# Kernel optimization log

Measured on AMD Instinct MI355X. Metric: run time of the kernel, lower is better.

Reference implementation:

```python
import jax, jax.numpy as jnp
import numpy as np

B, DIN, DOUT, K = 2048, 2048, 2048, 16

def setup_inputs() -> dict:
    key = jax.random.key(0)
    k1, k2, k3 = jax.random.split(key, 3)
    # init scale from reset_parameters: s = 3**0.5 / ((din+dout)/2 * k)**0.25
    d = (DIN + DOUT) / 2.0
    s = 3.0 ** 0.5 / (d * K) ** 0.25
    x = jax.random.normal(k1, (B, DIN), dtype=jnp.float32)
    w1 = jax.random.uniform(k2, (DIN, DOUT, K), minval=-s, maxval=s, dtype=jnp.float32)
    w2 = jax.random.uniform(k3, (DIN, DOUT, K), minval=-s, maxval=s, dtype=jnp.float32)
    b1 = jnp.zeros((DOUT, K), dtype=jnp.float32)
    b2 = jnp.zeros((DOUT,), dtype=jnp.float32)
    return {"x": x, "w1": w1, "b1": b1, "w2": w2, "b2": b2}

def reference(x, w1, b1, w2, b2):
    # g: [b, o, k] gating mixture, relu-activated
    g = jax.nn.relu(jnp.einsum('bi,iok->bok', x, w1) + b1)
    # three-way contraction over i and k -> [b, o]
    out = jnp.einsum('bi,iok,bok->bo', x, w2, g) + b2
    return out
```

## Files before the change

### kernel.cpp

```cpp
#include <hip/hip_runtime.h>
#include <hip/hip_bf16.h>


typedef __bf16 bf16;
typedef bf16 bf16x8 __attribute__((ext_vector_type(8)));
typedef bf16 bf16x4 __attribute__((ext_vector_type(4)));
typedef float f32x4 __attribute__((ext_vector_type(4)));

typedef __attribute__((address_space(1))) const void gco_void;
typedef __attribute__((address_space(3))) void lds_void;

#define DIN_   2048
#define DOUT_  2048
#define NP_    32768

__device__ __forceinline__ bf16x8 cvt8(f32x4 a, f32x4 b) {
    bf16x8 v;
    v[0] = (bf16)a[0]; v[1] = (bf16)a[1]; v[2] = (bf16)a[2]; v[3] = (bf16)a[3];
    v[4] = (bf16)b[0]; v[5] = (bf16)b[1]; v[6] = (bf16)b[2]; v[7] = (bf16)b[3];
    return v;
}

__global__ __launch_bounds__(256)
void xcvt(const float* __restrict__ x, bf16* __restrict__ xb) {
    const size_t i = ((size_t)blockIdx.x * 256 + threadIdx.x) * 8;
    f32x4 a = *(const f32x4*)(x + i);
    f32x4 b = *(const f32x4*)(x + i + 4);
    *(bf16x8*)(xb + i) = cvt8(a, b);
}

__global__ __launch_bounds__(256)
void wtrans(const float* __restrict__ w1, const float* __restrict__ w2,
            bf16* __restrict__ w1t, bf16* __restrict__ w2t) {
    __shared__ float s[64][65];
    const int t  = threadIdx.x;
    const int lr = t >> 4;
    const int lq = t & 15;
    const int n0 = blockIdx.x * 64;
    const int i0 = blockIdx.y * 64;
    const float* src = blockIdx.z ? w2 : w1;
    bf16*        dst = blockIdx.z ? w2t : w1t;
#pragma unroll
    for (int r = 0; r < 4; ++r) {
        const int il = lr + 16 * r;
        f32x4 v = *(const f32x4*)(src + (size_t)(i0 + il) * NP_ + n0 + lq * 4);
        s[il][lq * 4 + 0] = v[0]; s[il][lq * 4 + 1] = v[1];
        s[il][lq * 4 + 2] = v[2]; s[il][lq * 4 + 3] = v[3];
    }
    __syncthreads();
#pragma unroll
    for (int r = 0; r < 4; ++r) {
        const int nl = lr + 16 * r;
        bf16x4 o;
        o[0] = (bf16)s[lq * 4 + 0][nl]; o[1] = (bf16)s[lq * 4 + 1][nl];
        o[2] = (bf16)s[lq * 4 + 2][nl]; o[3] = (bf16)s[lq * 4 + 3][nl];
        *(bf16x4*)(dst + (size_t)(n0 + nl) * DIN_ + i0 + lq * 4) = o;
    }
}

__global__ __launch_bounds__(1024, 1)
void mix2_gemm16w(const bf16* __restrict__ xb, const bf16* __restrict__ w1t,
                  const bf16* __restrict__ w2t, const float* __restrict__ b1,
                  const float* __restrict__ b2, float* __restrict__ out)
{
    __shared__ alignas(16) char lds[131072];

    const int tid  = threadIdx.x;
    const int lane = tid & 63;
    const int wid  = tid >> 6;
    const int wm   = wid >> 2;
    const int wn   = wid & 3;
    const int lk   = lane & 15;
    const int lg   = lane >> 4;

    const int nwg = gridDim.x;
    const int bid = (blockIdx.x & 7) * (nwg >> 3) + (blockIdx.x >> 3);
    const int mt  = bid & 7;
    const int nt  = bid >> 3;

    const int arow = tid >> 2;
    const int aswz = ((tid & 3) ^ ((arow >> 1) & 3)) * 8;
    const int tb   = tid & 511;
    const int brow = tb >> 2;
    const int bswz = ((tb & 3) ^ ((brow >> 1) & 3)) * 8;
    const bf16* gA = xb + (size_t)(mt * 256 + arow) * DIN_ + aswz;
    const bf16* gB = (tid < 512 ? w1t : w2t) + (size_t)(nt * 128 + brow) * DIN_ + bswz;
    const int adst = arow * 64 + (tid & 3) * 16;
    const int bdst = 16384 + (tid >= 512 ? 8192 : 0) + tb * 16;

    const int kswz = (lg ^ ((lk >> 1) & 3)) * 16;
    int aoff[4], boff[2];
#pragma unroll
    for (int fm = 0; fm < 4; ++fm) aoff[fm] = (wm * 64 + fm * 16 + lk) * 64 + kswz;
#pragma unroll
    for (int fn = 0; fn < 2; ++fn) boff[fn] = 16384 + (wn * 32 + fn * 16 + lk) * 64 + kswz;

    f32x4 acc1[4][2], acc2[4][2];
#pragma unroll
    for (int i = 0; i < 4; ++i)
#pragma unroll
        for (int j = 0; j < 2; ++j) {
            acc1[i][j] = (f32x4){0.f, 0.f, 0.f, 0.f};
            acc2[i][j] = (f32x4){0.f, 0.f, 0.f, 0.f};
        }

    auto STG = [&](int h) {
        char* r = lds + (h & 3) * 32768;
        const int koff = h * 32;
        __builtin_amdgcn_global_load_lds((gco_void*)(gA + koff), (lds_void*)(r + adst), 16, 0, 0);
        __builtin_amdgcn_global_load_lds((gco_void*)(gB + koff), (lds_void*)(r + bdst), 16, 0, 0);
    };

    auto PHASE = [&](int h) {
        const char* r = lds + (h & 3) * 32768;
        bf16x8 a[4], u[2], v[2];
#pragma unroll
        for (int fn = 0; fn < 2; ++fn) {
            u[fn] = *(const bf16x8*)(r + boff[fn]);
            v[fn] = *(const bf16x8*)(r + boff[fn] + 8192);
        }
#pragma unroll
        for (int fm = 0; fm < 4; ++fm) a[fm] = *(const bf16x8*)(r + aoff[fm]);
        __builtin_amdgcn_s_setprio(1);
#pragma unroll
        for (int fm = 0; fm < 4; ++fm)
#pragma unroll
            for (int fn = 0; fn < 2; ++fn) {
                acc1[fm][fn] = __builtin_amdgcn_mfma_f32_16x16x32_bf16(a[fm], u[fn], acc1[fm][fn], 0, 0, 0);
                acc2[fm][fn] = __builtin_amdgcn_mfma_f32_16x16x32_bf16(a[fm], v[fn], acc2[fm][fn], 0, 0, 0);
            }
        __builtin_amdgcn_s_setprio(0);
    };

#define SYNC(W) do { asm volatile("s_waitcnt vmcnt(" #W ")" ::: "memory"); \
    __builtin_amdgcn_s_barrier(); __builtin_amdgcn_sched_barrier(0); } while (0)

    STG(0); STG(1); STG(2);

#pragma unroll 1
    for (int t = 0; t < 15; ++t) {
        const int h0 = t * 4;
#pragma unroll
        for (int q = 0; q < 4; ++q) {
            SYNC(4);
            STG(h0 + q + 3);
            PHASE(h0 + q);
        }
    }
    SYNC(4); STG(63); PHASE(60);
    SYNC(4);          PHASE(61);
    SYNC(2);          PHASE(62);
    SYNC(0);          PHASE(63);

#undef SYNC

    const int obase = nt * 8 + wn * 2;
#pragma unroll
    for (int fn = 0; fn < 2; ++fn) {
        const int o = obase + fn;
        const float bb1 = b1[(size_t)o * 16 + lk];
        const float bb2 = b2[o];
#pragma unroll
        for (int fm = 0; fm < 4; ++fm) {
#pragma unroll
            for (int j = 0; j < 4; ++j) {
                float g = fmaxf(acc1[fm][fn][j] + bb1, 0.f);
                float p = g * acc2[fm][fn][j];
                p += __shfl_xor(p, 1);
                p += __shfl_xor(p, 2);
                p += __shfl_xor(p, 4);
                p += __shfl_xor(p, 8);
                if (lk == 0) {
                    const int brow2 = mt * 256 + wm * 64 + fm * 16 + lg * 4 + j;
                    out[(size_t)brow2 * DOUT_ + o] = p + bb2;
                }
            }
        }
    }
}

__global__ __launch_bounds__(512)
void mix2_fused_direct(const float* __restrict__ x, const float* __restrict__ w1,
                       const float* __restrict__ b1, const float* __restrict__ w2,
                       const float* __restrict__ b2, float* __restrict__ out)
{
    __shared__ alignas(16) char lds[2 * 49152];

    const int tid  = threadIdx.x;
    const int lane = tid & 63;
    const int wid  = tid >> 6;
    const int wm   = wid >> 2;
    const int wn   = wid & 3;

    const int nwg = gridDim.x;
    const int bid = (blockIdx.x & 7) * (nwg >> 3) + (blockIdx.x >> 3);
    const int mt  = bid & 15;
    const int nt  = bid >> 4;

    const int lk  = lane & 15;
    const int lg  = lane >> 4;
    const int swz = (lane & 7) << 4;

    const int a_row  = tid >> 3;
    const int a_col8 = tid & 7;
    const int b_ib = ((tid >> 5) & 15) << 2;
    const int b_nb = (tid & 31) << 2;

    const float* pa  = x  + (size_t)(mt * 128 + a_row) * DIN_ + a_col8 * 8;
    const float* pb1 = w1 + (size_t)b_ib * NP_ + (size_t)nt * 128 + b_nb;
    const float* pb2 = w2 + (size_t)b_ib * NP_ + (size_t)nt * 128 + b_nb;

    const int aswz   = (a_col8 * 16) ^ ((a_row & 7) << 4);
    const int aoffw0 = a_row * 128 + aswz;
    const int aoffw1 = (a_row + 64) * 128 + aswz;

    int aoff[4], boff1[2], boff2[2];
#pragma unroll
    for (int fm = 0; fm < 4; ++fm) aoff[fm] = (wm * 64 + fm * 16 + lk) * 128;
#pragma unroll
    for (int fn = 0; fn < 2; ++fn) {
        const int n = wn * 32 + fn * 16 + lk;
        boff1[fn] = 16384 + n * 128;
        boff2[fn] = 32768 + n * 128;
    }
    const int kp0 = (lg * 16) ^ swz;
    const int kp1 = (64 + lg * 16) ^ swz;

    f32x4 acc1[4][2], acc2[4][2];
#pragma unroll
    for (int i = 0; i < 4; ++i)
#pragma unroll
        for (int j = 0; j < 2; ++j) {
            acc1[i][j] = (f32x4){0.f, 0.f, 0.f, 0.f};
            acc2[i][j] = (f32x4){0.f, 0.f, 0.f, 0.f};
        }

    f32x4 rA[4], rB1[4], rB2[4];

    auto LOAD = [&](int kt) {
        const float* a0 = pa + kt * 64;
        rA[0] = *(const f32x4*)(a0);
        rA[1] = *(const f32x4*)(a0 + 4);
        rA[2] = *(const f32x4*)(a0 + (size_t)64 * DIN_);
        rA[3] = *(const f32x4*)(a0 + (size_t)64 * DIN_ + 4);
        const float* q1 = pb1 + (size_t)kt * 64 * NP_;
        const float* q2 = pb2 + (size_t)kt * 64 * NP_;
#pragma unroll
        for (int j = 0; j < 4; ++j) {
            rB1[j] = *(const f32x4*)(q1 + (size_t)j * NP_);
            rB2[j] = *(const f32x4*)(q2 + (size_t)j * NP_);
        }
    };

    auto STORE = [&](char* s) {
        *(bf16x8*)(s + aoffw0) = cvt8(rA[0], rA[1]);
        *(bf16x8*)(s + aoffw1) = cvt8(rA[2], rA[3]);
        char* s1 = s + 16384;
        char* s2 = s + 32768;
#pragma unroll
        for (int c = 0; c < 4; ++c) {
            const int n   = b_nb + c;
            const int off = n * 128 + ((b_ib * 2) ^ ((n & 7) << 4));
            bf16x4 v1, v2;
            v1[0] = (bf16)rB1[0][c]; v1[1] = (bf16)rB1[1][c];
            v1[2] = (bf16)rB1[2][c]; v1[3] = (bf16)rB1[3][c];
            v2[0] = (bf16)rB2[0][c]; v2[1] = (bf16)rB2[1][c];
            v2[2] = (bf16)rB2[2][c]; v2[3] = (bf16)rB2[3][c];
            *(bf16x4*)(s1 + off) = v1;
            *(bf16x4*)(s2 + off) = v2;
        }
    };

    auto COMPUTE = [&](const char* s) {
#pragma unroll
        for (int kb = 0; kb < 2; ++kb) {
            const int kp = kb ? kp1 : kp0;
            bf16x8 a[4], u[2], v[2];
#pragma unroll
            for (int fm = 0; fm < 4; ++fm) a[fm] = *(const bf16x8*)(s + aoff[fm] + kp);
#pragma unroll
            for (int fn = 0; fn < 2; ++fn) u[fn] = *(const bf16x8*)(s + boff1[fn] + kp);
#pragma unroll
            for (int fn = 0; fn < 2; ++fn) v[fn] = *(const bf16x8*)(s + boff2[fn] + kp);
#pragma unroll
            for (int fm = 0; fm < 4; ++fm)
#pragma unroll
                for (int fn = 0; fn < 2; ++fn) {
                    acc1[fm][fn] = __builtin_amdgcn_mfma_f32_16x16x32_bf16(a[fm], u[fn], acc1[fm][fn], 0, 0, 0);
                    acc2[fm][fn] = __builtin_amdgcn_mfma_f32_16x16x32_bf16(a[fm], v[fn], acc2[fm][fn], 0, 0, 0);
                }
        }
    };

    char* buf0 = lds;
    char* buf1 = lds + 49152;

    LOAD(0);
    STORE(buf0);
    __syncthreads();

    for (int kt = 0; kt < 32; ++kt) {
        if (kt + 1 < 32) LOAD(kt + 1);
        COMPUTE((kt & 1) ? buf1 : buf0);
        if (kt + 1 < 32) {
            STORE((kt & 1) ? buf0 : buf1);
            __syncthreads();
        }
    }

    const int obase = nt * 8 + wn * 2;
#pragma unroll
    for (int fn = 0; fn < 2; ++fn) {
        const int o = obase + fn;
        const float bb1 = b1[(size_t)o * 16 + lk];
        const float bb2 = b2[o];
#pragma unroll
        for (int fm = 0; fm < 4; ++fm) {
#pragma unroll
            for (int j = 0; j < 4; ++j) {
                float g = fmaxf(acc1[fm][fn][j] + bb1, 0.f);
                float p = g * acc2[fm][fn][j];
                p += __shfl_xor(p, 1);
                p += __shfl_xor(p, 2);
                p += __shfl_xor(p, 4);
                p += __shfl_xor(p, 8);
                if (lk == 0) {
                    const int brow = mt * 128 + wm * 64 + fm * 16 + lg * 4 + j;
                    out[(size_t)brow * DOUT_ + o] = p + bb2;
                }
            }
        }
    }
}

extern "C" void kernel_launch(void* const* d_in, const int* in_sizes, int n_in,
                              void* d_out, int out_size, void* d_ws, size_t ws_size,
                              hipStream_t stream) {
    (void)in_sizes; (void)n_in; (void)out_size;
    const float* x  = (const float*)d_in[0];
    const float* w1 = (const float*)d_in[1];
    const float* b1 = (const float*)d_in[2];
    const float* w2 = (const float*)d_in[3];
    const float* b2 = (const float*)d_in[4];
    float* out = (float*)d_out;

    const size_t XB   = (size_t)DIN_ * DIN_ * 2;
    const size_t WT   = (size_t)NP_ * DIN_ * 2;
    const size_t NEED = XB + 2 * WT;

    if (ws_size >= NEED) {
        bf16* xb  = (bf16*)d_ws;
        bf16* w1t = (bf16*)((char*)d_ws + XB);
        bf16* w2t = (bf16*)((char*)d_ws + XB + WT);
        hipLaunchKernelGGL(xcvt,   dim3(2048),        dim3(256),  0, stream, x, xb);
        hipLaunchKernelGGL(wtrans, dim3(512, 32, 2),  dim3(256),  0, stream, w1, w2, w1t, w2t);
        hipLaunchKernelGGL(mix2_gemm16w, dim3(2048),  dim3(1024), 0, stream, xb, w1t, w2t, b1, b2, out);
    } else {
        hipLaunchKernelGGL(mix2_fused_direct, dim3(4096), dim3(512), 0, stream, x, w1, b1, w2, b2, out);
    }
}
```

Baseline: 642.8 us.

## Switch GEMM pipeline to double-buffered 64-wide K stages with full waits

Replaces the 4-stage ring of 32-wide K tiles (prefetch depth 3, partial vmcnt waits) with a 2-buffer scheme of 64-wide K tiles, each thread issuing four global-to-LDS loads per stage. It also uses a new 8-way XOR swizzle for the 128-byte rows. The goal is half as many barriers and more MFMA work per synchronisation. In exchange, prefetch depth drops to one stage and every stage waits on vmcnt(0), which may expose more memory latency.

```diff
diff --git a/kernel.cpp b/kernel.cpp
--- a/kernel.cpp
+++ b/kernel.cpp
@@ -59,9 +59,9 @@
 }
 
 __global__ __launch_bounds__(1024, 1)
-void mix2_gemm16w(const bf16* __restrict__ xb, const bf16* __restrict__ w1t,
-                  const bf16* __restrict__ w2t, const float* __restrict__ b1,
-                  const float* __restrict__ b2, float* __restrict__ out)
+void mix2_gemm2b(const bf16* __restrict__ xb, const bf16* __restrict__ w1t,
+                 const bf16* __restrict__ w2t, const float* __restrict__ b1,
+                 const float* __restrict__ b2, float* __restrict__ out)
 {
     __shared__ alignas(16) char lds[131072];
 
@@ -78,22 +78,28 @@
     const int mt  = bid & 7;
     const int nt  = bid >> 3;
 
-    const int arow = tid >> 2;
-    const int aswz = ((tid & 3) ^ ((arow >> 1) & 3)) * 8;
-    const int tb   = tid & 511;
-    const int brow = tb >> 2;
-    const int bswz = ((tb & 3) ^ ((brow >> 1) & 3)) * 8;
-    const bf16* gA = xb + (size_t)(mt * 256 + arow) * DIN_ + aswz;
-    const bf16* gB = (tid < 512 ? w1t : w2t) + (size_t)(nt * 128 + brow) * DIN_ + bswz;
-    const int adst = arow * 64 + (tid & 3) * 16;
-    const int bdst = 16384 + (tid >= 512 ? 8192 : 0) + tb * 16;
-
-    const int kswz = (lg ^ ((lk >> 1) & 3)) * 16;
-    int aoff[4], boff[2];
-#pragma unroll
-    for (int fm = 0; fm < 4; ++fm) aoff[fm] = (wm * 64 + fm * 16 + lk) * 64 + kswz;
-#pragma unroll
-    for (int fn = 0; fn < 2; ++fn) boff[fn] = 16384 + (wn * 32 + fn * 16 + lk) * 64 + kswz;
+    const int srow = tid >> 3;
+    const int sswz = ((tid & 7) ^ (srow & 7)) * 8;
+    const bf16* gA0 = xb  + (size_t)(mt * 256 + srow) * DIN_ + sswz;
+    const bf16* gA1 = gA0 + (size_t)128 * DIN_;
+    const bf16* gB1 = w1t + (size_t)(nt * 128 + srow) * DIN_ + sswz;
+    const bf16* gB2 = w2t + (size_t)(nt * 128 + srow) * DIN_ + sswz;
+
+    int aoff[4][2], boff[2][2];
+#pragma unroll
+    for (int fm = 0; fm < 4; ++fm)
+#pragma unroll
+        for (int h2 = 0; h2 < 2; ++h2) {
+            const int row = wm * 64 + fm * 16 + lk;
+            aoff[fm][h2] = row * 128 + (((h2 * 4 + lg) ^ (row & 7)) << 4);
+        }
+#pragma unroll
+    for (int fn = 0; fn < 2; ++fn)
+#pragma unroll
+        for (int h2 = 0; h2 < 2; ++h2) {
+            const int row = wn * 32 + fn * 16 + lk;
+            boff[fn][h2] = 32768 + row * 128 + (((h2 * 4 + lg) ^ (row & 7)) << 4);
+        }
 
     f32x4 acc1[4][2], acc2[4][2];
 #pragma unroll
@@ -104,53 +110,54 @@
             acc2[i][j] = (f32x4){0.f, 0.f, 0.f, 0.f};
         }
 
-    auto STG = [&](int h) {
-        char* r = lds + (h & 3) * 32768;
-        const int koff = h * 32;
-        __builtin_amdgcn_global_load_lds((gco_void*)(gA + koff), (lds_void*)(r + adst), 16, 0, 0);
-        __builtin_amdgcn_global_load_lds((gco_void*)(gB + koff), (lds_void*)(r + bdst), 16, 0, 0);
-    };
-
-    auto PHASE = [&](int h) {
-        const char* r = lds + (h & 3) * 32768;
-        bf16x8 a[4], u[2], v[2];
-#pragma unroll
-        for (int fn = 0; fn < 2; ++fn) {
-            u[fn] = *(const bf16x8*)(r + boff[fn]);
-            v[fn] = *(const bf16x8*)(r + boff[fn] + 8192);
-        }
-#pragma unroll
-        for (int fm = 0; fm < 4; ++fm) a[fm] = *(const bf16x8*)(r + aoff[fm]);
-        __builtin_amdgcn_s_setprio(1);
-#pragma unroll
-        for (int fm = 0; fm < 4; ++fm)
+    auto STG = [&](int t) {
+        char* r = lds + (t & 1) * 65536;
+        const int koff = t * 64;
+        __builtin_amdgcn_global_load_lds((gco_void*)(gA0 + koff), (lds_void*)(r + tid * 16),          16, 0, 0);
+        __builtin_amdgcn_global_load_lds((gco_void*)(gA1 + koff), (lds_void*)(r + 16384 + tid * 16),  16, 0, 0);
+        __builtin_amdgcn_global_load_lds((gco_void*)(gB1 + koff), (lds_void*)(r + 32768 + tid * 16),  16, 0, 0);
+        __builtin_amdgcn_global_load_lds((gco_void*)(gB2 + koff), (lds_void*)(r + 49152 + tid * 16),  16, 0, 0);
+    };
+
+    auto COMPUTE = [&](const char* r) {
+#pragma unroll
+        for (int h2 = 0; h2 < 2; ++h2) {
+            bf16x8 a[4], u[2], v[2];
 #pragma unroll
             for (int fn = 0; fn < 2; ++fn) {
-                acc1[fm][fn] = __builtin_amdgcn_mfma_f32_16x16x32_bf16(a[fm], u[fn], acc1[fm][fn], 0, 0, 0);
-                acc2[fm][fn] = __builtin_amdgcn_mfma_f32_16x16x32_bf16(a[fm], v[fn], acc2[fm][fn], 0, 0, 0);
+                u[fn] = *(const bf16x8*)(r + boff[fn][h2]);
+                v[fn] = *(const bf16x8*)(r + boff[fn][h2] + 16384);
             }
-        __builtin_amdgcn_s_setprio(0);
-    };
-
-#define SYNC(W) do { asm volatile("s_waitcnt vmcnt(" #W ")" ::: "memory"); \
+#pragma unroll
+            for (int fm = 0; fm < 4; ++fm) a[fm] = *(const bf16x8*)(r + aoff[fm][h2]);
+            __builtin_amdgcn_s_setprio(1);
+#pragma unroll
+            for (int fm = 0; fm < 4; ++fm)
+#pragma unroll
+                for (int fn = 0; fn < 2; ++fn) {
+                    acc1[fm][fn] = __builtin_amdgcn_mfma_f32_16x16x32_bf16(a[fm], u[fn], acc1[fm][fn], 0, 0, 0);
+                    acc2[fm][fn] = __builtin_amdgcn_mfma_f32_16x16x32_bf16(a[fm], v[fn], acc2[fm][fn], 0, 0, 0);
+                }
+            __builtin_amdgcn_s_setprio(0);
+        }
+    };
+
+#define SYNC() do { asm volatile("s_waitcnt vmcnt(0)" ::: "memory"); \
     __builtin_amdgcn_s_barrier(); __builtin_amdgcn_sched_barrier(0); } while (0)
 
-    STG(0); STG(1); STG(2);
+    const char* buf0 = lds;
+    const char* buf1 = lds + 65536;
+
+    STG(0);
 
 #pragma unroll 1
-    for (int t = 0; t < 15; ++t) {
-        const int h0 = t * 4;
-#pragma unroll
-        for (int q = 0; q < 4; ++q) {
-            SYNC(4);
-            STG(h0 + q + 3);
-            PHASE(h0 + q);
-        }
-    }
-    SYNC(4); STG(63); PHASE(60);
-    SYNC(4);          PHASE(61);
-    SYNC(2);          PHASE(62);
-    SYNC(0);          PHASE(63);
+    for (int tt = 0; tt < 15; ++tt) {
+        const int t = tt * 2;
+        SYNC(); STG(t + 1); COMPUTE(buf0);
+        SYNC(); STG(t + 2); COMPUTE(buf1);
+    }
+    SYNC(); STG(31); COMPUTE(buf0);
+    SYNC();          COMPUTE(buf1);
 
 #undef SYNC
 
@@ -171,8 +178,8 @@
                 p += __shfl_xor(p, 4);
                 p += __shfl_xor(p, 8);
                 if (lk == 0) {
-                    const int brow2 = mt * 256 + wm * 64 + fm * 16 + lg * 4 + j;
-                    out[(size_t)brow2 * DOUT_ + o] = p + bb2;
+                    const int brow = mt * 256 + wm * 64 + fm * 16 + lg * 4 + j;
+                    out[(size_t)brow * DOUT_ + o] = p + bb2;
                 }
             }
         }
@@ -352,9 +359,9 @@
         bf16* xb  = (bf16*)d_ws;
         bf16* w1t = (bf16*)((char*)d_ws + XB);
         bf16* w2t = (bf16*)((char*)d_ws + XB + WT);
-        hipLaunchKernelGGL(xcvt,   dim3(2048),        dim3(256),  0, stream, x, xb);
-        hipLaunchKernelGGL(wtrans, dim3(512, 32, 2),  dim3(256),  0, stream, w1, w2, w1t, w2t);
-        hipLaunchKernelGGL(mix2_gemm16w, dim3(2048),  dim3(1024), 0, stream, xb, w1t, w2t, b1, b2, out);
+        hipLaunchKernelGGL(xcvt,   dim3(2048),       dim3(256),  0, stream, x, xb);
+        hipLaunchKernelGGL(wtrans, dim3(512, 32, 2), dim3(256),  0, stream, w1, w2, w1t, w2t);
+        hipLaunchKernelGGL(mix2_gemm2b, dim3(2048),  dim3(1024), 0, stream, xb, w1t, w2t, b1, b2, out);
     } else {
         hipLaunchKernelGGL(mix2_fused_direct, dim3(4096), dim3(512), 0, stream, x, w1, b1, w2, b2, out);
     }
```

Result: no change. 634.3 us (-1.3%).
